# Performance work log

Hardware: AMD Instinct MI355X
Metric: run time of the kernel (lower is better)

The kernel has to match this reference:

```python
import jax, jax.numpy as jnp
import numpy as np

N_NODES = 100000
N_EDGES = 1000000
HIDDEN = 128
N_GRAPHS = 256
EPS = 1e-6
LN_EPS = 1e-5


def _normalize(x, eps=1e-12):
    n = jnp.linalg.norm(x, axis=-1, keepdims=True)
    return x / jnp.maximum(n, eps)


def _shiftl(b, k):
    # boolean shift-left by k (positions idx-k in the torch code)
    return jnp.concatenate([b[k:], jnp.zeros((k,), dtype=bool)])


def _quaternions(R):
    Rxx, Ryy, Rzz = R[:, 0, 0], R[:, 1, 1], R[:, 2, 2]
    mag = 0.5 * jnp.sqrt(jnp.abs(1.0 + jnp.stack([Rxx - Ryy - Rzz, -Rxx + Ryy - Rzz, -Rxx - Ryy + Rzz], -1)))
    signs = jnp.sign(jnp.stack([R[:, 2, 1] - R[:, 1, 2], R[:, 0, 2] - R[:, 2, 0], R[:, 1, 0] - R[:, 0, 1]], -1))
    w = jnp.sqrt(jax.nn.relu(1.0 + Rxx + Ryy + Rzz))[:, None] / 2.0
    return _normalize(jnp.concatenate([signs * mag, w], -1))


def _layer_norm(x, g, b):
    m = jnp.mean(x, -1, keepdims=True)
    v = jnp.mean((x - m) ** 2, -1, keepdims=True)
    return (x - m) / jnp.sqrt(v + LN_EPS) * g + b


def _forward(X, batch, edge_index, W_node, b_node, g_node, beta_node, W_edge, b_edge, g_edge, beta_edge):
    N = X.shape[0]
    # bnd[i] True iff node i starts a new graph (torch: idx positions that get NaN-masked)
    bnd = jnp.concatenate([jnp.zeros((1,), dtype=bool), batch[1:] != batch[:-1]])

    # ---- dihedrals over consecutive central atoms ----
    U = _normalize(X[1:] - X[:-1])                               # [N-1,3]
    c1 = _normalize(jnp.cross(U[:-2], U[1:-1]))
    c2 = _normalize(jnp.cross(U[1:-1], U[2:]))
    cosd = jnp.clip(jnp.sum(c1 * c2, -1), -1.0 + EPS, 1.0 - EPS)
    dih = jnp.arccos(cosd) * jnp.sign(jnp.sum(c2 * U[:-2], -1))  # [N-3]
    dih = jnp.pad(dih, (1, 2))                                   # [N]; pads are masked below
    bad_d = (bnd | _shiftl(bnd, 1) | _shiftl(bnd, 2)).at[jnp.array([0, N - 2, N - 1])].set(True)
    dihedral = jnp.where(bad_d[:, None], 0.0, jnp.stack([jnp.sin(dih), jnp.cos(dih)], -1))  # [N,2]

    # ---- bond angles ----
    d0 = _normalize(X[:-2] - X[1:-1])
    d1 = _normalize(X[2:] - X[1:-1])
    cosa = jnp.sum(d0 * d1, -1)
    sina = jnp.sqrt(1.0 - cosa ** 2 + EPS)
    bad_a = (bnd | _shiftl(bnd, 1)).at[jnp.array([0, N - 1])].set(True)
    angle = jnp.where(bad_a[:, None], 0.0,
                      jnp.stack([jnp.pad(sina, (1, 1)), jnp.pad(cosa, (1, 1))], -1))        # [N,2]

    # ---- local frames Q (same invalid set as angles: idx, idx-1, 0, N-1) ----
    bvec = _normalize(U[:-1] - U[1:])
    nvec = _normalize(jnp.cross(U[:-1], U[1:]))
    Q = jnp.stack([bvec, nvec, jnp.cross(bvec, nvec)], -1)       # [N-2,3,3]
    Q = jnp.pad(Q, ((1, 1), (0, 0), (0, 0)))                     # [N,3,3]
    Q = jnp.where(bad_a[:, None, None], 0.0, Q)
    valid = ~bad_a

    # ---- edge features (gather-heavy) ----
    src, tgt = edge_index[0], edge_index[1]
    src_Q, tgt_Q = Q[src], Q[tgt]                                # [E,3,3]
    R = jnp.einsum('eji,ejk->eik', tgt_Q, src_Q)                 # tgt_Q^T @ src_Q
    orient = jnp.where((valid[src] & valid[tgt])[:, None], _quaternions(R), 0.0)            # [E,4]

    dvec = X[src] - X[tgt]
    dist = jnp.sqrt(jnp.sum(dvec ** 2, -1) + EPS)
    mu = jnp.linspace(0.0, 20.0, 16)                             # D_min=0, D_max=20, num_rbf=16
    rbf = jnp.exp(-(((dist[:, None] - mu) * (16.0 / 20.0)) ** 2))                            # [E,16]

    direct = jnp.einsum('eji,ej->ei', tgt_Q, _normalize(dvec))
    direct = jnp.where(valid[tgt][:, None], direct, 0.0)                                     # [E,3]

    h_V = jnp.concatenate([dihedral, angle], -1)                 # [N,4]
    h_E = jnp.concatenate([orient, rbf, direct], -1)             # [E,23]
    h_V = _layer_norm(h_V @ W_node + b_node, g_node, beta_node)
    h_E = _layer_norm(h_E @ W_edge + b_edge, g_edge, beta_edge)
    return h_V, h_E


def setup_inputs() -> dict:
    key = jax.random.key(0)
    ks = jax.random.split(key, 8)
    central_coords = jax.random.normal(ks[0], (N_NODES, 3), jnp.float32) * 3.0
    batch = jnp.sort(jax.random.randint(ks[1], (N_NODES,), 0, N_GRAPHS))
    edge_index = jax.random.randint(ks[2], (2, N_EDGES), 0, N_NODES)
    W_node = jax.random.normal(ks[3], (4, HIDDEN), jnp.float32) * 0.5
    b_node = jax.random.normal(ks[4], (HIDDEN,), jnp.float32) * 0.02
    W_edge = jax.random.normal(ks[5], (23, HIDDEN), jnp.float32) * 0.2
    b_edge = jax.random.normal(ks[6], (HIDDEN,), jnp.float32) * 0.02
    return dict(central_coords=central_coords, batch=batch, edge_index=edge_index,
                W_node=W_node, b_node=b_node,
                g_node=jnp.ones((HIDDEN,), jnp.float32), beta_node=jnp.zeros((HIDDEN,), jnp.float32),
                W_edge=W_edge, b_edge=b_edge,
                g_edge=jnp.ones((HIDDEN,), jnp.float32), beta_edge=jnp.zeros((HIDDEN,), jnp.float32))


def reference(central_coords, batch, edge_index, W_node, b_node, g_node, beta_node, W_edge, b_edge, g_edge, beta_edge):
    return _forward(central_coords, batch, edge_index, W_node, b_node, g_node, beta_node, W_edge, b_edge, g_edge, beta_edge)
```

## Files before the change

kernel.cpp:

```cpp
#include <hip/hip_runtime.h>
#include <math.h>

struct V3 { float x, y, z; };
__device__ __forceinline__ V3 v3(float a, float b, float c){ V3 r; r.x=a; r.y=b; r.z=c; return r; }
__device__ __forceinline__ V3 vsub(V3 a, V3 b){ return v3(a.x-b.x, a.y-b.y, a.z-b.z); }
__device__ __forceinline__ float vdot(V3 a, V3 b){ return a.x*b.x + a.y*b.y + a.z*b.z; }
__device__ __forceinline__ V3 vcross(V3 a, V3 b){
  return v3(a.y*b.z - a.z*b.y, a.z*b.x - a.x*b.z, a.x*b.y - a.y*b.x);
}
__device__ __forceinline__ V3 vunit(V3 a){
  float n = sqrtf(vdot(a,a));
  float inv = 1.0f / fmaxf(n, 1e-12f);
  return v3(a.x*inv, a.y*inv, a.z*inv);
}
__device__ __forceinline__ float sgnf(float x){ return (x > 0.f) ? 1.f : ((x < 0.f) ? -1.f : 0.f); }
__device__ __forceinline__ float bcastf(float v, int lane){
  return __int_as_float(__builtin_amdgcn_readlane(__float_as_int(v), lane));
}

__global__ void setup_gram(const float* __restrict__ Wn, const float* __restrict__ bn,
                           const float* __restrict__ We, const float* __restrict__ be,
                           float* __restrict__ Ge, float* __restrict__ abarE,
                           float* __restrict__ Gn, float* __restrict__ abarN)
{
  int tid = threadIdx.x;
  if (tid < 576) {
    int i = tid / 24, j = tid % 24;
    const float* ai = (i < 23) ? (We + i * 128) : be;
    const float* aj = (j < 23) ? (We + j * 128) : be;
    float s = 0.f;
    for (int c = 0; c < 128; ++c) s += ai[c] * aj[c];
    Ge[tid] = s * (1.0f / 128.0f);
  } else if (tid < 601) {
    int t = tid - 576; int i = t / 5, j = t % 5;
    const float* ai = (i < 4) ? (Wn + i * 128) : bn;
    const float* aj = (j < 4) ? (Wn + j * 128) : bn;
    float s = 0.f;
    for (int c = 0; c < 128; ++c) s += ai[c] * aj[c];
    Gn[t] = s * (1.0f / 128.0f);
  } else if (tid < 625) {
    int k = tid - 601;
    const float* a = (k < 23) ? (We + k * 128) : be;
    float s = 0.f;
    for (int c = 0; c < 128; ++c) s += a[c];
    abarE[k] = s * (1.0f / 128.0f);
  } else if (tid < 630) {
    int k = tid - 625;
    const float* a = (k < 4) ? (Wn + k * 128) : bn;
    float s = 0.f;
    for (int c = 0; c < 128; ++c) s += a[c];
    abarN[k] = s * (1.0f / 128.0f);
  }
}

__global__ __launch_bounds__(256) void node_kernel(
    const float* __restrict__ X, const int* __restrict__ batch,
    const float* __restrict__ Wn, const float* __restrict__ bn,
    const float* __restrict__ gn, const float* __restrict__ betan,
    const float* __restrict__ Gn, const float* __restrict__ abarN,
    float* __restrict__ Qws, int* __restrict__ validws,
    float* __restrict__ outV, int N)
{
  int lane = threadIdx.x & 63;
  int wave = threadIdx.x >> 6;
  int base = blockIdx.x * 256 + wave * 64;
  int i = base + lane;
  bool live = (i < N);
  int ic = live ? i : (N - 1);

  int im1 = (ic >= 1) ? ic - 1 : 0;
  int ip1 = (ic + 1 < N) ? ic + 1 : N - 1;
  int ip2 = (ic + 2 < N) ? ic + 2 : N - 1;

  V3 xm1 = v3(X[3*im1], X[3*im1+1], X[3*im1+2]);
  V3 x0  = v3(X[3*ic ], X[3*ic +1], X[3*ic +2]);
  V3 xp1 = v3(X[3*ip1], X[3*ip1+1], X[3*ip1+2]);
  V3 xp2 = v3(X[3*ip2], X[3*ip2+1], X[3*ip2+2]);

  int b0 = batch[ic];
  bool bnd_i  = (ic >= 1)    && (batch[ic - 1] != b0);
  bool bnd_i1 = (ic + 1 < N) && (batch[ic + 1] != b0);
  bool bnd_i2 = (ic + 2 < N) && (batch[ic + 2] != batch[ic + 1]);

  bool bad_d = bnd_i || bnd_i1 || bnd_i2 || (ic == 0) || (ic >= N - 2);
  bool bad_a = bnd_i || bnd_i1 || (ic == 0) || (ic == N - 1);

  V3 u0 = vunit(vsub(x0,  xm1));
  V3 u1 = vunit(vsub(xp1, x0 ));
  V3 u2 = vunit(vsub(xp2, xp1));
  V3 c1 = vunit(vcross(u0, u1));
  V3 c2 = vunit(vcross(u1, u2));

  float cosd = vdot(c1, c2);
  cosd = fminf(fmaxf(cosd, -1.0f + 1e-6f), 1.0f - 1e-6f);
  float sd = vdot(c2, u0);
  float f0, f1;
  if (bad_d)          { f0 = 0.f; f1 = 0.f; }
  else {
    float sg = sgnf(sd);
    if (sg == 0.f)    { f0 = 0.f; f1 = 1.f; }
    else              { f0 = sg * sqrtf(fmaxf(1.f - cosd * cosd, 0.f)); f1 = cosd; }
  }

  V3 d0 = vunit(vsub(xm1, x0));
  V3 d1 = vunit(vsub(xp1, x0));
  float cosa = vdot(d0, d1);
  float sina = sqrtf(fmaxf(1.0f - cosa * cosa + 1e-6f, 0.f));
  float f2 = bad_a ? 0.f : sina;
  float f3 = bad_a ? 0.f : cosa;

  V3 bv = vunit(vsub(u0, u1));
  V3 nv = c1;
  V3 tv = vcross(bv, nv);
  float q[9];
  if (bad_a) {
    #pragma unroll
    for (int k = 0; k < 9; ++k) q[k] = 0.f;
  } else {
    q[0]=bv.x; q[1]=nv.x; q[2]=tv.x;
    q[3]=bv.y; q[4]=nv.y; q[5]=tv.y;
    q[6]=bv.z; q[7]=nv.z; q[8]=tv.z;
  }
  if (live) {
    #pragma unroll
    for (int k = 0; k < 9; ++k) Qws[(size_t)i * 9 + k] = q[k];
    validws[i] = bad_a ? 0 : 1;
  }

  float fa[5] = { f0, f1, f2, f3, 1.0f };
  float mmean = 0.f;
  #pragma unroll
  for (int k = 0; k < 5; ++k) mmean = fmaf(fa[k], abarN[k], mmean);
  float E2 = 0.f;
  #pragma unroll
  for (int ii = 0; ii < 5; ++ii) {
    float ti = 0.f;
    #pragma unroll
    for (int jj = 0; jj < 5; ++jj) ti = fmaf(Gn[ii * 5 + jj], fa[jj], ti);
    E2 = fmaf(fa[ii], ti, E2);
  }
  float var  = fmaxf(E2 - mmean * mmean, 0.f);
  float rstd = rsqrtf(var + 1e-5f);

  float W0[4], W1[4];
  #pragma unroll
  for (int k = 0; k < 4; ++k) { W0[k] = Wn[k * 128 + lane]; W1[k] = Wn[k * 128 + 64 + lane]; }
  float c_b0 = bn[lane],    c_b1 = bn[64 + lane];
  float c_g0 = gn[lane],    c_g1 = gn[64 + lane];
  float c_e0 = betan[lane], c_e1 = betan[64 + lane];

  for (int t = 0; t < 64; ++t) {
    int node = base + t;
    if (node >= N) break;
    float bf0 = bcastf(f0, t), bf1 = bcastf(f1, t);
    float bf2 = bcastf(f2, t), bf3 = bcastf(f3, t);
    float bm  = bcastf(mmean, t), br = bcastf(rstd, t);
    float y0 = c_b0, y1 = c_b1;
    y0 = fmaf(bf0, W0[0], y0); y0 = fmaf(bf1, W0[1], y0);
    y0 = fmaf(bf2, W0[2], y0); y0 = fmaf(bf3, W0[3], y0);
    y1 = fmaf(bf0, W1[0], y1); y1 = fmaf(bf1, W1[1], y1);
    y1 = fmaf(bf2, W1[2], y1); y1 = fmaf(bf3, W1[3], y1);
    size_t ro = (size_t)node * 128;
    outV[ro + lane]      = (y0 - bm) * br * c_g0 + c_e0;
    outV[ro + 64 + lane] = (y1 - bm) * br * c_g1 + c_e1;
  }
}

__global__ __launch_bounds__(256) void edge_kernel(
    const float* __restrict__ X, const int* __restrict__ eidx,
    const float* __restrict__ We, const float* __restrict__ be,
    const float* __restrict__ ge, const float* __restrict__ betae,
    const float* __restrict__ Qws, const int* __restrict__ validws,
    const float* __restrict__ Ge, const float* __restrict__ abarE,
    float* __restrict__ outE, int N, int E)
{
  int lane = threadIdx.x & 63;
  int wave = threadIdx.x >> 6;
  int base = blockIdx.x * 256 + wave * 64;
  int e = base + lane;
  int ec = (e < E) ? e : (E - 1);

  int s = eidx[ec];
  int t = eidx[E + ec];

  float Xs0 = X[3*s], Xs1 = X[3*s+1], Xs2 = X[3*s+2];
  float Xt0 = X[3*t], Xt1 = X[3*t+1], Xt2 = X[3*t+2];

  float Qs[9], Qt[9];
  #pragma unroll
  for (int k = 0; k < 9; ++k) { Qs[k] = Qws[(size_t)s * 9 + k]; Qt[k] = Qws[(size_t)t * 9 + k]; }
  int ok = validws[s] & validws[t];

  float R[9];
  #pragma unroll
  for (int i = 0; i < 3; ++i) {
    #pragma unroll
    for (int k = 0; k < 3; ++k) {
      R[3*i+k] = Qt[i] * Qs[k] + Qt[3+i] * Qs[3+k] + Qt[6+i] * Qs[6+k];
    }
  }

  float Rxx = R[0], Ryy = R[4], Rzz = R[8];
  float m0 = 0.5f * sqrtf(fabsf(1.f + Rxx - Ryy - Rzz));
  float m1 = 0.5f * sqrtf(fabsf(1.f - Rxx + Ryy - Rzz));
  float m2 = 0.5f * sqrtf(fabsf(1.f - Rxx - Ryy + Rzz));
  float s0 = sgnf(R[7] - R[5]);
  float s1 = sgnf(R[2] - R[6]);
  float s2 = sgnf(R[3] - R[1]);
  float w  = 0.5f * sqrtf(fmaxf(1.f + Rxx + Ryy + Rzz, 0.f));
  float q0 = s0 * m0, q1 = s1 * m1, q2 = s2 * m2;
  float qn = fmaxf(sqrtf(q0*q0 + q1*q1 + q2*q2 + w*w), 1e-12f);
  float qinv = 1.0f / qn;
  float msk = ok ? 1.f : 0.f;

  float f[23];
  f[0] = q0 * qinv * msk; f[1] = q1 * qinv * msk;
  f[2] = q2 * qinv * msk; f[3] = w  * qinv * msk;

  float dx = Xs0 - Xt0, dy = Xs1 - Xt1, dz = Xs2 - Xt2;
  float d2 = dx*dx + dy*dy + dz*dz;
  float dist = sqrtf(d2 + 1e-6f);
  #pragma unroll
  for (int k = 0; k < 16; ++k) {
    float u = (dist - (float)k * (20.0f / 15.0f)) * 0.8f;
    f[4 + k] = __expf(-u * u);
  }
  float dn = fmaxf(sqrtf(d2), 1e-12f);
  float rinv = 1.0f / dn;
  float ux = dx * rinv, uy = dy * rinv, uz = dz * rinv;
  f[20] = Qt[0]*ux + Qt[3]*uy + Qt[6]*uz;
  f[21] = Qt[1]*ux + Qt[4]*uy + Qt[7]*uz;
  f[22] = Qt[2]*ux + Qt[5]*uy + Qt[8]*uz;

  float mmean = abarE[23];
  #pragma unroll
  for (int k = 0; k < 23; ++k) mmean = fmaf(f[k], abarE[k], mmean);
  float E2 = 0.f;
  #pragma unroll
  for (int ii = 0; ii < 24; ++ii) {
    float fi = (ii < 23) ? f[ii] : 1.0f;
    float ti = 0.f;
    #pragma unroll
    for (int jj = 0; jj < 24; ++jj) {
      float fj = (jj < 23) ? f[jj] : 1.0f;
      ti = fmaf(Ge[ii * 24 + jj], fj, ti);
    }
    E2 = fmaf(fi, ti, E2);
  }
  float var  = fmaxf(E2 - mmean * mmean, 0.f);
  float rstd = rsqrtf(var + 1e-5f);

  float W0[23], W1[23];
  #pragma unroll
  for (int k = 0; k < 23; ++k) { W0[k] = We[k * 128 + lane]; W1[k] = We[k * 128 + 64 + lane]; }
  float c_b0 = be[lane],    c_b1 = be[64 + lane];
  float c_g0 = ge[lane],    c_g1 = ge[64 + lane];
  float c_e0 = betae[lane], c_e1 = betae[64 + lane];

  for (int tt = 0; tt < 64; ++tt) {
    int ee = base + tt;
    if (ee >= E) break;
    float bm = bcastf(mmean, tt), br = bcastf(rstd, tt);
    float y0 = c_b0, y1 = c_b1;
    #pragma unroll
    for (int k = 0; k < 23; ++k) {
      float bf = bcastf(f[k], tt);
      y0 = fmaf(bf, W0[k], y0);
      y1 = fmaf(bf, W1[k], y1);
    }
    size_t ro = (size_t)ee * 128;
    outE[ro + lane]      = (y0 - bm) * br * c_g0 + c_e0;
    outE[ro + 64 + lane] = (y1 - bm) * br * c_g1 + c_e1;
  }
}

extern "C" void kernel_launch(void* const* d_in, const int* in_sizes, int n_in,
                              void* d_out, int out_size, void* d_ws, size_t ws_size,
                              hipStream_t stream)
{
  const float* X     = (const float*)d_in[0];
  const int*   batch = (const int*)  d_in[1];
  const int*   eidx  = (const int*)  d_in[2];
  const float* Wn    = (const float*)d_in[3];
  const float* bn    = (const float*)d_in[4];
  const float* gn    = (const float*)d_in[5];
  const float* betan = (const float*)d_in[6];
  const float* We    = (const float*)d_in[7];
  const float* be    = (const float*)d_in[8];
  const float* ge    = (const float*)d_in[9];
  const float* betae = (const float*)d_in[10];

  int N = in_sizes[0] / 3;
  int E = in_sizes[2] / 2;

  float* ws      = (float*)d_ws;
  float* Qws     = ws;
  int*   validws = (int*)(ws + (size_t)N * 9);
  float* Ge      = ws + (size_t)N * 9 + N;
  float* abarE   = Ge + 576;
  float* Gn      = abarE + 24;
  float* abarN   = Gn + 25;

  float* outV = (float*)d_out;
  float* outE = outV + (size_t)N * 128;

  hipLaunchKernelGGL(setup_gram, dim3(1), dim3(640), 0, stream,
                     Wn, bn, We, be, Ge, abarE, Gn, abarN);

  int nblocks = (N + 255) / 256;
  hipLaunchKernelGGL(node_kernel, dim3(nblocks), dim3(256), 0, stream,
                     X, batch, Wn, bn, gn, betan, Gn, abarN, Qws, validws, outV, N);

  int eblocks = (E + 255) / 256;
  hipLaunchKernelGGL(edge_kernel, dim3(eblocks), dim3(256), 0, stream,
                     X, eidx, We, be, ge, betae, Qws, validws, Ge, abarE, outE, N, E);
}
```

Baseline: 722.8 us.

## Pack node frame with coords, stage edge features in LDS, vectorize output stores

Each node's 9-float frame is now stored together with its coordinates in a 12-float record, so an edge gathers each endpoint with three 16-byte loads instead of many scalar loads from two arrays. The edge kernel writes per-edge features, mean and rstd to rotated shared-memory rows and reads them back as vec4, replacing per-feature readlane broadcasts. Each lane now owns two adjacent output columns and writes them as one float2 store. The cost is 32KB of LDS per block, which can limit occupancy, plus an extra block barrier.

```diff
diff --git a/kernel.cpp b/kernel.cpp
--- a/kernel.cpp
+++ b/kernel.cpp
@@ -1,5 +1,8 @@
 #include <hip/hip_runtime.h>
 #include <math.h>
+
+typedef __attribute__((ext_vector_type(2))) float f32x2;
+typedef __attribute__((ext_vector_type(4))) float f32x4;
 
 struct V3 { float x, y, z; };
 __device__ __forceinline__ V3 v3(float a, float b, float c){ V3 r; r.x=a; r.y=b; r.z=c; return r; }
@@ -122,8 +125,11 @@
     q[6]=bv.z; q[7]=nv.z; q[8]=tv.z;
   }
   if (live) {
-    #pragma unroll
-    for (int k = 0; k < 9; ++k) Qws[(size_t)i * 9 + k] = q[k];
+    f32x4* qp = (f32x4*)(Qws + (size_t)i * 12);
+    f32x4 ca; ca.x=q[0]; ca.y=q[1]; ca.z=q[2]; ca.w=q[3];
+    f32x4 cb; cb.x=q[4]; cb.y=q[5]; cb.z=q[6]; cb.w=q[7];
+    f32x4 cc; cc.x=q[8]; cc.y=x0.x; cc.z=x0.y; cc.w=x0.z;
+    qp[0] = ca; qp[1] = cb; qp[2] = cc;
     validws[i] = bad_a ? 0 : 1;
   }
 
@@ -142,12 +148,12 @@
   float var  = fmaxf(E2 - mmean * mmean, 0.f);
   float rstd = rsqrtf(var + 1e-5f);
 
-  float W0[4], W1[4];
-  #pragma unroll
-  for (int k = 0; k < 4; ++k) { W0[k] = Wn[k * 128 + lane]; W1[k] = Wn[k * 128 + 64 + lane]; }
-  float c_b0 = bn[lane],    c_b1 = bn[64 + lane];
-  float c_g0 = gn[lane],    c_g1 = gn[64 + lane];
-  float c_e0 = betan[lane], c_e1 = betan[64 + lane];
+  f32x2 W2[4];
+  #pragma unroll
+  for (int k = 0; k < 4; ++k) W2[k] = *(const f32x2*)(Wn + k * 128 + 2 * lane);
+  f32x2 b2 = *(const f32x2*)(bn    + 2 * lane);
+  f32x2 g2 = *(const f32x2*)(gn    + 2 * lane);
+  f32x2 e2 = *(const f32x2*)(betan + 2 * lane);
 
   for (int t = 0; t < 64; ++t) {
     int node = base + t;
@@ -155,25 +161,29 @@
     float bf0 = bcastf(f0, t), bf1 = bcastf(f1, t);
     float bf2 = bcastf(f2, t), bf3 = bcastf(f3, t);
     float bm  = bcastf(mmean, t), br = bcastf(rstd, t);
-    float y0 = c_b0, y1 = c_b1;
-    y0 = fmaf(bf0, W0[0], y0); y0 = fmaf(bf1, W0[1], y0);
-    y0 = fmaf(bf2, W0[2], y0); y0 = fmaf(bf3, W0[3], y0);
-    y1 = fmaf(bf0, W1[0], y1); y1 = fmaf(bf1, W1[1], y1);
-    y1 = fmaf(bf2, W1[2], y1); y1 = fmaf(bf3, W1[3], y1);
-    size_t ro = (size_t)node * 128;
-    outV[ro + lane]      = (y0 - bm) * br * c_g0 + c_e0;
-    outV[ro + 64 + lane] = (y1 - bm) * br * c_g1 + c_e1;
+    f32x2 acc = b2;
+    f32x2 s0 = bf0, s1 = bf1, s2 = bf2, s3 = bf3;
+    acc = __builtin_elementwise_fma(s0, W2[0], acc);
+    acc = __builtin_elementwise_fma(s1, W2[1], acc);
+    acc = __builtin_elementwise_fma(s2, W2[2], acc);
+    acc = __builtin_elementwise_fma(s3, W2[3], acc);
+    f32x2 out;
+    out.x = (acc.x - bm) * br * g2.x + e2.x;
+    out.y = (acc.y - bm) * br * g2.y + e2.y;
+    *(f32x2*)(outV + (size_t)node * 128 + 2 * lane) = out;
   }
 }
 
 __global__ __launch_bounds__(256) void edge_kernel(
-    const float* __restrict__ X, const int* __restrict__ eidx,
+    const int* __restrict__ eidx,
     const float* __restrict__ We, const float* __restrict__ be,
     const float* __restrict__ ge, const float* __restrict__ betae,
     const float* __restrict__ Qws, const int* __restrict__ validws,
     const float* __restrict__ Ge, const float* __restrict__ abarE,
     float* __restrict__ outE, int N, int E)
 {
+  __shared__ float smem[256 * 32];
+
   int lane = threadIdx.x & 63;
   int wave = threadIdx.x >> 6;
   int base = blockIdx.x * 256 + wave * 64;
@@ -183,12 +193,15 @@
   int s = eidx[ec];
   int t = eidx[E + ec];
 
-  float Xs0 = X[3*s], Xs1 = X[3*s+1], Xs2 = X[3*s+2];
-  float Xt0 = X[3*t], Xt1 = X[3*t+1], Xt2 = X[3*t+2];
-
-  float Qs[9], Qt[9];
-  #pragma unroll
-  for (int k = 0; k < 9; ++k) { Qs[k] = Qws[(size_t)s * 9 + k]; Qt[k] = Qws[(size_t)t * 9 + k]; }
+  const f32x4* sp = (const f32x4*)(Qws + (size_t)s * 12);
+  const f32x4* tp = (const f32x4*)(Qws + (size_t)t * 12);
+  f32x4 sA = sp[0], sB = sp[1], sC = sp[2];
+  f32x4 tA = tp[0], tB = tp[1], tC = tp[2];
+
+  float Qs[9] = { sA.x, sA.y, sA.z, sA.w, sB.x, sB.y, sB.z, sB.w, sC.x };
+  float Qt[9] = { tA.x, tA.y, tA.z, tA.w, tB.x, tB.y, tB.z, tB.w, tC.x };
+  float Xs0 = sC.y, Xs1 = sC.z, Xs2 = sC.w;
+  float Xt0 = tC.y, Xt1 = tC.z, Xt2 = tC.w;
   int ok = validws[s] & validws[t];
 
   float R[9];
@@ -250,27 +263,51 @@
   float var  = fmaxf(E2 - mmean * mmean, 0.f);
   float rstd = rsqrtf(var + 1e-5f);
 
-  float W0[23], W1[23];
-  #pragma unroll
-  for (int k = 0; k < 23; ++k) { W0[k] = We[k * 128 + lane]; W1[k] = We[k * 128 + 64 + lane]; }
-  float c_b0 = be[lane],    c_b1 = be[64 + lane];
-  float c_g0 = ge[lane],    c_g1 = ge[64 + lane];
-  float c_e0 = betae[lane], c_e1 = betae[64 + lane];
-
+  {
+    float ch[28];
+    #pragma unroll
+    for (int k = 0; k < 23; ++k) ch[k] = f[k];
+    ch[23] = mmean; ch[24] = rstd; ch[25] = 0.f; ch[26] = 0.f; ch[27] = 0.f;
+    f32x4* rowp = (f32x4*)(smem + (int)threadIdx.x * 32);
+    int rot = lane & 7;
+    #pragma unroll
+    for (int c = 0; c < 7; ++c) {
+      f32x4 v; v.x = ch[4*c]; v.y = ch[4*c+1]; v.z = ch[4*c+2]; v.w = ch[4*c+3];
+      rowp[(c + rot) & 7] = v;
+    }
+  }
+  __syncthreads();
+
+  f32x2 Wc[23];
+  #pragma unroll
+  for (int k = 0; k < 23; ++k) Wc[k] = *(const f32x2*)(We + k * 128 + 2 * lane);
+  f32x2 b2 = *(const f32x2*)(be    + 2 * lane);
+  f32x2 g2 = *(const f32x2*)(ge    + 2 * lane);
+  f32x2 e2 = *(const f32x2*)(betae + 2 * lane);
+
+  #pragma unroll 2
   for (int tt = 0; tt < 64; ++tt) {
     int ee = base + tt;
     if (ee >= E) break;
-    float bm = bcastf(mmean, tt), br = bcastf(rstd, tt);
-    float y0 = c_b0, y1 = c_b1;
+    const f32x4* rp = (const f32x4*)(smem + (wave * 64 + tt) * 32);
+    int rot2 = tt & 7;
+    float fs[28];
+    #pragma unroll
+    for (int c = 0; c < 7; ++c) {
+      f32x4 v = rp[(c + rot2) & 7];
+      fs[4*c] = v.x; fs[4*c+1] = v.y; fs[4*c+2] = v.z; fs[4*c+3] = v.w;
+    }
+    float bm = fs[23], br = fs[24];
+    f32x2 acc = b2;
     #pragma unroll
     for (int k = 0; k < 23; ++k) {
-      float bf = bcastf(f[k], tt);
-      y0 = fmaf(bf, W0[k], y0);
-      y1 = fmaf(bf, W1[k], y1);
-    }
-    size_t ro = (size_t)ee * 128;
-    outE[ro + lane]      = (y0 - bm) * br * c_g0 + c_e0;
-    outE[ro + 64 + lane] = (y1 - bm) * br * c_g1 + c_e1;
+      f32x2 sv = fs[k];
+      acc = __builtin_elementwise_fma(sv, Wc[k], acc);
+    }
+    f32x2 out;
+    out.x = (acc.x - bm) * br * g2.x + e2.x;
+    out.y = (acc.y - bm) * br * g2.y + e2.y;
+    *(f32x2*)(outE + (size_t)ee * 128 + 2 * lane) = out;
   }
 }
 
@@ -295,8 +332,8 @@
 
   float* ws      = (float*)d_ws;
   float* Qws     = ws;
-  int*   validws = (int*)(ws + (size_t)N * 9);
-  float* Ge      = ws + (size_t)N * 9 + N;
+  int*   validws = (int*)(ws + (size_t)N * 12);
+  float* Ge      = ws + (size_t)N * 12 + N;
   float* abarE   = Ge + 576;
   float* Gn      = abarE + 24;
   float* abarN   = Gn + 25;
@@ -313,5 +350,5 @@
 
   int eblocks = (E + 255) / 256;
   hipLaunchKernelGGL(edge_kernel, dim3(eblocks), dim3(256), 0, stream,
-                     X, eidx, We, be, ge, betae, Qws, validws, Ge, abarE, outE, N, E);
-}
+                     eidx, We, be, ge, betae, Qws, validws, Ge, abarE, outE, N, E);
+}
```

New measurement: 645.7 us. -10.7%, faster.
